# Kernel optimization log

Measured on AMD Instinct MI355X. Metric: run time of the kernel, lower is better.

## Reference

```python
import jax, jax.numpy as jnp
import numpy as np

NBINS = 256


def setup_inputs() -> dict:
    key = jax.random.key(0)
    x = jax.random.uniform(key, (16, 3, 1024, 1024), dtype=jnp.float32)
    return {"x": x}


def reference(x):
    b, c, h, w = x.shape
    n = b * c
    xf = x.reshape(n, h * w)                      # (n, N) per-channel rows

    # global min/max over the whole tensor (matches torch.histogram range)
    mn = xf.min()
    mx = xf.max()
    span = mx - mn

    # per-row histogram via scatter-add; last bin is right-closed like torch.histogram
    scale = NBINS / span
    idx = jnp.clip(jnp.floor((xf - mn) * scale).astype(jnp.int32), 0, NBINS - 1)
    flat_idx = (jnp.arange(n, dtype=jnp.int32)[:, None] * NBINS + idx).reshape(-1)
    hist = jax.ops.segment_sum(
        jnp.ones((n * h * w,), dtype=jnp.float32), flat_idx,
        num_segments=n * NBINS,
    ).reshape(n, NBINS)
    hist = hist / hist.sum(axis=1, keepdims=True)  # normalized histograms

    # vectorized Otsu: cumulative weights/means -> inter-class variance
    t = jnp.arange(NBINS, dtype=hist.dtype)
    w_bg = jnp.cumsum(hist, axis=1)               # background weight up to t
    s_bg = jnp.cumsum(hist * t, axis=1)           # background weighted sum
    total = s_bg[:, -1:]                          # sum_i i*hist[i]
    w_fg = 1.0 - w_bg
    valid = (w_bg > 0) & (w_fg > 0)
    mean_bg = s_bg / jnp.where(w_bg > 0, w_bg, 1.0)
    mean_fg = (total - s_bg) / jnpp_safe(w_fg) if False else (total - s_bg) / jnp.where(w_fg > 0, w_fg, 1.0)
    var = jnp.where(valid, w_bg * w_fg * (mean_bg - mean_fg) ** 2, -jnp.inf)
    t_opt = jnp.argmax(var, axis=1)               # first max, like strict `>` loop

    # threshold = right edge of the optimal bin
    edges = mn + span * (jnp.arange(NBINS + 1, dtype=x.dtype) / NBINS)
    thresh = edges[t_opt + 1]                     # (n,)

    out = jnp.where(xf <= thresh[:, None], jnp.zeros((), x.dtype), xf)
    return out.reshape(b, c, h, w)
```

## Files before the change

### kernel.cpp

```cpp
#include <hip/hip_runtime.h>
#include <stdint.h>

#define NBINS 256
#define HW_SHIFT 20
#define HW4_SHIFT (HW_SHIFT-2)
#define BLK_PER_IMG 64

__device__ __forceinline__ unsigned enc_f(float f) {
    unsigned u = __float_as_uint(f);
    return (u & 0x80000000u) ? ~u : (u | 0x80000000u);
}
__device__ __forceinline__ float dec_f(unsigned e) {
    unsigned u = (e & 0x80000000u) ? (e ^ 0x80000000u) : ~e;
    return __uint_as_float(u);
}

__global__ void k_init(unsigned* mmo, unsigned* hist, int nhist) {
    int t = threadIdx.x + blockIdx.x * blockDim.x;
    if (t == 0) { mmo[0] = 0xFFFFFFFFu; mmo[1] = 0u; }
    for (int i = t; i < nhist; i += blockDim.x * gridDim.x) hist[i] = 0u;
}

__global__ void k_minmax(const float4* __restrict__ x, unsigned* mmo, long n4) {
    unsigned mn = 0xFFFFFFFFu, mx = 0u;
    long stride = (long)gridDim.x * blockDim.x;
    for (long i = (long)blockIdx.x * blockDim.x + threadIdx.x; i < n4; i += stride) {
        float4 v = x[i];
        unsigned e0 = enc_f(v.x), e1 = enc_f(v.y), e2 = enc_f(v.z), e3 = enc_f(v.w);
        mn = min(mn, min(min(e0, e1), min(e2, e3)));
        mx = max(mx, max(max(e0, e1), max(e2, e3)));
    }
    for (int off = 32; off > 0; off >>= 1) {
        mn = min(mn, (unsigned)__shfl_down((int)mn, off));
        mx = max(mx, (unsigned)__shfl_down((int)mx, off));
    }
    __shared__ unsigned smn[4], smx[4];
    int lane = threadIdx.x & 63, w = threadIdx.x >> 6;
    if (lane == 0) { smn[w] = mn; smx[w] = mx; }
    __syncthreads();
    if (threadIdx.x == 0) {
        for (int j = 1; j < (int)(blockDim.x >> 6); j++) {
            mn = min(mn, smn[j]); mx = max(mx, smx[j]);
        }
        atomicMin(&mmo[0], mn);
        atomicMax(&mmo[1], mx);
    }
}

__global__ void k_hist(const float4* __restrict__ x, const unsigned* __restrict__ mmo,
                       unsigned* __restrict__ ghist) {
    __shared__ unsigned sh[NBINS];
    for (int i = threadIdx.x; i < NBINS; i += blockDim.x) sh[i] = 0u;
    __syncthreads();
    float mn = dec_f(mmo[0]);
    float mx = dec_f(mmo[1]);
    float span = mx - mn;
    float scale = __fdiv_rn(256.0f, span);
    int img = blockIdx.x / BLK_PER_IMG;
    int blk = blockIdx.x % BLK_PER_IMG;
    const float4* base = x + ((long)img << HW4_SHIFT);
    const int n4i = 1 << HW4_SHIFT;
    for (int i = blk * blockDim.x + threadIdx.x; i < n4i; i += BLK_PER_IMG * blockDim.x) {
        float4 v = base[i];
        int b0 = (int)floorf((v.x - mn) * scale);
        int b1 = (int)floorf((v.y - mn) * scale);
        int b2 = (int)floorf((v.z - mn) * scale);
        int b3 = (int)floorf((v.w - mn) * scale);
        b0 = min(max(b0, 0), NBINS - 1);
        b1 = min(max(b1, 0), NBINS - 1);
        b2 = min(max(b2, 0), NBINS - 1);
        b3 = min(max(b3, 0), NBINS - 1);
        atomicAdd(&sh[b0], 1u);
        atomicAdd(&sh[b1], 1u);
        atomicAdd(&sh[b2], 1u);
        atomicAdd(&sh[b3], 1u);
    }
    __syncthreads();
    for (int i = threadIdx.x; i < NBINS; i += blockDim.x) {
        unsigned c = sh[i];
        if (c) atomicAdd(&ghist[img * NBINS + i], c);
    }
}

__global__ void k_otsu(const unsigned* __restrict__ ghist, const unsigned* __restrict__ mmo,
                       float* __restrict__ thresh, int nimg) {
    int i = threadIdx.x + blockIdx.x * blockDim.x;
    if (i >= nimg) return;
    const unsigned* h = ghist + i * NBINS;
    const float inv_total = 1.0f / 1048576.0f;
    float w = 0.0f, s = 0.0f;
    for (int t = 0; t < NBINS; t++) {
        float p = __fmul_rn((float)h[t], inv_total);
        w = __fadd_rn(w, p);
        s = __fadd_rn(s, __fmul_rn(p, (float)t));
    }
    float total = s;
    float best = -__builtin_inff();
    int bestt = 0;
    w = 0.0f; s = 0.0f;
    for (int t = 0; t < NBINS; t++) {
        float p = __fmul_rn((float)h[t], inv_total);
        w = __fadd_rn(w, p);
        s = __fadd_rn(s, __fmul_rn(p, (float)t));
        float wf = __fsub_rn(1.0f, w);
        float var;
        if (w > 0.0f && wf > 0.0f) {
            float mb = __fdiv_rn(s, w);
            float mf = __fdiv_rn(__fsub_rn(total, s), wf);
            float d = __fsub_rn(mb, mf);
            var = __fmul_rn(__fmul_rn(w, wf), __fmul_rn(d, d));
        } else {
            var = -__builtin_inff();
        }
        if (var > best) { best = var; bestt = t; }
    }
    float mn = dec_f(mmo[0]);
    float mx = dec_f(mmo[1]);
    float span = __fsub_rn(mx, mn);
    float q = __fmul_rn((float)(bestt + 1), 1.0f / 256.0f);
    thresh[i] = __fadd_rn(mn, __fmul_rn(span, q));
}

__global__ void k_apply(const float4* __restrict__ x, float4* __restrict__ out,
                        const float* __restrict__ thresh, long n4) {
    long stride = (long)gridDim.x * blockDim.x;
    for (long i = (long)blockIdx.x * blockDim.x + threadIdx.x; i < n4; i += stride) {
        int img = (int)(i >> HW4_SHIFT);
        float th = thresh[img];
        float4 v = x[i];
        float4 o;
        o.x = (v.x <= th) ? 0.0f : v.x;
        o.y = (v.y <= th) ? 0.0f : v.y;
        o.z = (v.z <= th) ? 0.0f : v.z;
        o.w = (v.w <= th) ? 0.0f : v.w;
        out[i] = o;
    }
}

extern "C" void kernel_launch(void* const* d_in, const int* in_sizes, int n_in,
                              void* d_out, int out_size, void* d_ws, size_t ws_size,
                              hipStream_t stream) {
    const float* x = (const float*)d_in[0];
    float* out = (float*)d_out;
    long n = (long)in_sizes[0];
    long n4 = n >> 2;
    int nimg = (int)(n >> HW_SHIFT);

    unsigned* mmo = (unsigned*)d_ws;
    unsigned* ghist = mmo + 2;
    float* thresh = (float*)(ghist + nimg * NBINS);

    k_init<<<48, 256, 0, stream>>>(mmo, ghist, nimg * NBINS);
    k_minmax<<<2048, 256, 0, stream>>>((const float4*)x, mmo, n4);
    k_hist<<<nimg * BLK_PER_IMG, 256, 0, stream>>>((const float4*)x, mmo, ghist);
    k_otsu<<<1, 64, 0, stream>>>(ghist, mmo, thresh, nimg);
    k_apply<<<4096, 256, 0, stream>>>((const float4*)x, (float4*)out, thresh, n4);
}
```

Measured before the change: 483.6 us.

## Privatize shared histogram into 32 copies, stage Otsu in LDS, nontemporal output stores

The shared-memory histogram is replicated into 32 lane-indexed copies so that atomics from threads hitting the same bin no longer contend, and the copies are reduced per bin at the end. The Otsu kernel now loads all histograms into padded LDS with 256 threads before the per-image scan, which avoids strided global reads. The apply kernel writes its output with nontemporal stores, and the float sign encoding becomes branchless. The costs are 32 KB of LDS per histogram block, which may lower occupancy, and a hardcoded LDS size of 48 images in the Otsu kernel.

```diff
diff --git a/kernel.cpp b/kernel.cpp
--- a/kernel.cpp
+++ b/kernel.cpp
@@ -5,10 +5,13 @@
 #define HW_SHIFT 20
 #define HW4_SHIFT (HW_SHIFT-2)
 #define BLK_PER_IMG 64
+#define NCOPY 32
+
+typedef float nfloat4 __attribute__((ext_vector_type(4)));
 
 __device__ __forceinline__ unsigned enc_f(float f) {
     unsigned u = __float_as_uint(f);
-    return (u & 0x80000000u) ? ~u : (u | 0x80000000u);
+    return u ^ ((unsigned)((int)u >> 31) | 0x80000000u);
 }
 __device__ __forceinline__ float dec_f(unsigned e) {
     unsigned u = (e & 0x80000000u) ? (e ^ 0x80000000u) : ~e;
@@ -49,8 +52,8 @@
 
 __global__ void k_hist(const float4* __restrict__ x, const unsigned* __restrict__ mmo,
                        unsigned* __restrict__ ghist) {
-    __shared__ unsigned sh[NBINS];
-    for (int i = threadIdx.x; i < NBINS; i += blockDim.x) sh[i] = 0u;
+    __shared__ unsigned sh[NBINS * NCOPY];
+    for (int i = threadIdx.x; i < NBINS * NCOPY; i += blockDim.x) sh[i] = 0u;
     __syncthreads();
     float mn = dec_f(mmo[0]);
     float mx = dec_f(mmo[1]);
@@ -60,6 +63,7 @@
     int blk = blockIdx.x % BLK_PER_IMG;
     const float4* base = x + ((long)img << HW4_SHIFT);
     const int n4i = 1 << HW4_SHIFT;
+    int c = threadIdx.x & (NCOPY - 1);
     for (int i = blk * blockDim.x + threadIdx.x; i < n4i; i += BLK_PER_IMG * blockDim.x) {
         float4 v = base[i];
         int b0 = (int)floorf((v.x - mn) * scale);
@@ -70,23 +74,34 @@
         b1 = min(max(b1, 0), NBINS - 1);
         b2 = min(max(b2, 0), NBINS - 1);
         b3 = min(max(b3, 0), NBINS - 1);
-        atomicAdd(&sh[b0], 1u);
-        atomicAdd(&sh[b1], 1u);
-        atomicAdd(&sh[b2], 1u);
-        atomicAdd(&sh[b3], 1u);
+        atomicAdd(&sh[b0 * NCOPY + c], 1u);
+        atomicAdd(&sh[b1 * NCOPY + c], 1u);
+        atomicAdd(&sh[b2 * NCOPY + c], 1u);
+        atomicAdd(&sh[b3 * NCOPY + c], 1u);
     }
     __syncthreads();
-    for (int i = threadIdx.x; i < NBINS; i += blockDim.x) {
-        unsigned c = sh[i];
-        if (c) atomicAdd(&ghist[img * NBINS + i], c);
+    int bin = threadIdx.x;
+    unsigned sum = 0;
+    #pragma unroll
+    for (int k = 0; k < NCOPY; k++) {
+        int cc = (k + threadIdx.x) & (NCOPY - 1);
+        sum += sh[bin * NCOPY + cc];
     }
+    if (sum) atomicAdd(&ghist[img * NBINS + bin], sum);
 }
 
 __global__ void k_otsu(const unsigned* __restrict__ ghist, const unsigned* __restrict__ mmo,
                        float* __restrict__ thresh, int nimg) {
-    int i = threadIdx.x + blockIdx.x * blockDim.x;
+    __shared__ unsigned sh[48 * (NBINS + 1)];
+    int total_h = nimg * NBINS;
+    for (int i = threadIdx.x; i < total_h; i += blockDim.x) {
+        int im = i >> 8, b = i & 255;
+        sh[im * (NBINS + 1) + b] = ghist[i];
+    }
+    __syncthreads();
+    int i = threadIdx.x;
     if (i >= nimg) return;
-    const unsigned* h = ghist + i * NBINS;
+    const unsigned* h = sh + i * (NBINS + 1);
     const float inv_total = 1.0f / 1048576.0f;
     float w = 0.0f, s = 0.0f;
     for (int t = 0; t < NBINS; t++) {
@@ -121,19 +136,19 @@
     thresh[i] = __fadd_rn(mn, __fmul_rn(span, q));
 }
 
-__global__ void k_apply(const float4* __restrict__ x, float4* __restrict__ out,
+__global__ void k_apply(const float4* __restrict__ x, nfloat4* __restrict__ out,
                         const float* __restrict__ thresh, long n4) {
     long stride = (long)gridDim.x * blockDim.x;
     for (long i = (long)blockIdx.x * blockDim.x + threadIdx.x; i < n4; i += stride) {
         int img = (int)(i >> HW4_SHIFT);
         float th = thresh[img];
         float4 v = x[i];
-        float4 o;
+        nfloat4 o;
         o.x = (v.x <= th) ? 0.0f : v.x;
         o.y = (v.y <= th) ? 0.0f : v.y;
         o.z = (v.z <= th) ? 0.0f : v.z;
         o.w = (v.w <= th) ? 0.0f : v.w;
-        out[i] = o;
+        __builtin_nontemporal_store(o, &out[i]);
     }
 }
 
@@ -153,6 +168,6 @@
     k_init<<<48, 256, 0, stream>>>(mmo, ghist, nimg * NBINS);
     k_minmax<<<2048, 256, 0, stream>>>((const float4*)x, mmo, n4);
     k_hist<<<nimg * BLK_PER_IMG, 256, 0, stream>>>((const float4*)x, mmo, ghist);
-    k_otsu<<<1, 64, 0, stream>>>(ghist, mmo, thresh, nimg);
-    k_apply<<<4096, 256, 0, stream>>>((const float4*)x, (float4*)out, thresh, n4);
+    k_otsu<<<1, 256, 0, stream>>>(ghist, mmo, thresh, nimg);
+    k_apply<<<4096, 256, 0, stream>>>((const float4*)x, (nfloat4*)out, thresh, n4);
 }
```

Measured after the change: 476.7 us. No clear change (-1.4%).
